# Optimization experiments

Hardware: AMD Instinct MI355X
Metric: run time of the kernel (lower is better)

## Reference

```python
import jax, jax.numpy as jnp
import numpy as np

B, M, K, D = 16384, 16, 256, 64
T = 1.0


def setup_inputs() -> dict:
    key = jax.random.key(0)
    k1, k2 = jax.random.split(key)
    x = jax.random.normal(k1, (B, M, D), dtype=jnp.float32)
    # nn.init.normal_(self.center, std=0.01)
    center = jax.random.normal(k2, (M, K, D), dtype=jnp.float32) * 0.01
    return {"x": x, "center": center}


def _forward(x, center):
    # x: [B, M, D]; center: [M, K, D]
    x1 = jax.lax.stop_gradient(x)              # x.detach() in the original
    x_sqlen = jnp.sum(x1 * x1, axis=-1)        # [B, M]
    dot = jnp.einsum('mkd,bmd->bmk', center, x1)  # bmm(center, x1) -> [B, M, K]
    c_sqlen = jnp.sum(center * center, axis=-1)   # [M, K]
    dist = c_sqlen[None, :, :] - 2.0 * dot + x_sqlen[:, :, None]  # [B, M, K]
    dist = -jnp.sqrt(dist)
    # softargmax with straight-through estimator
    y_soft = jax.nn.softmax(dist / T, axis=-1)
    label = jnp.argmax(y_soft, axis=-1, keepdims=True)            # [B, M, 1]
    y_hard = jax.nn.one_hot(label[..., 0], K, dtype=dist.dtype)   # [B, M, K]
    assign = y_hard - jax.lax.stop_gradient(y_soft) + y_soft
    # reconstruction: bmm(assign^T(M,B,K), center(M,K,D)) -> [B, M, D]
    recon = jnp.einsum('bmk,mkd->bmd', assign, center)
    return recon, center, label


def reference(x, center):
    return _forward(x, center)
```

## Files before the change

### kernel.cpp

```cpp
#include <hip/hip_runtime.h>
#include <stdint.h>
#include <math.h>

#define B_TOT 16384
#define M_TOT 16
#define K_TOT 256
#define D_TOT 64
#define ROWS_PB 256
#define THREADS 512
#define NCHUNK (B_TOT / ROWS_PB)
#define CAP 3072
#define XS 8.0e-3f
#define SLACK 5.0e-5f

typedef unsigned long long ull;
typedef __attribute__((ext_vector_type(8))) short short8;
typedef __attribute__((ext_vector_type(4))) float f32x4;
typedef __attribute__((ext_vector_type(4))) uint32_t u32x4;

__device__ __forceinline__ uint32_t f32_key(float f) {
  uint32_t u = __float_as_uint(f);
  return (u & 0x80000000u) ? ~u : (u | 0x80000000u);
}
__device__ __forceinline__ ull u64min(ull a, ull b) { return a < b ? a : b; }

__device__ __forceinline__ uint32_t bf16rne(float f) {
  uint32_t u = __float_as_uint(f);
  return (u + 0x7FFFu + ((u >> 16) & 1u)) >> 16;
}
__device__ __forceinline__ uint32_t pack2(float a, float b) {
  return bf16rne(a) | (bf16rne(b) << 16);
}

__device__ __forceinline__ int swz(int row, int c) {
  return row * 128 + ((c * 16) ^ ((row & 7) << 4));
}

__device__ __forceinline__ float xla_hsum16(const float* r) {
#pragma clang fp contract(off)
#pragma clang fp reassociate(off)
  float u[8];
#pragma unroll
  for (int q = 0; q < 8; ++q) u[q] = r[q] + r[q + 8];
  float v[4];
#pragma unroll
  for (int q = 0; q < 4; ++q) v[q] = u[q] + u[q + 4];
  float w0 = v[0] + v[2];
  float w1 = v[1] + v[3];
  return w0 + w1;
}

__device__ __forceinline__ ull exact_key_stream(int k, const float* __restrict__ xrow,
                                                const float* __restrict__ crow,
                                                float csq, float x_sq) {
#pragma clang fp contract(off)
#pragma clang fp reassociate(off)
  const float4* cp = reinterpret_cast<const float4*>(crow);
  const float4* xp = reinterpret_cast<const float4*>(xrow);
  float a[4] = {0.f, 0.f, 0.f, 0.f};
#pragma unroll
  for (int it = 0; it < 4; ++it) {
    float cc[16], xx[16];
#pragma unroll
    for (int q = 0; q < 4; ++q) {
      float4 v = cp[4 * it + q];
      cc[4 * q + 0] = v.x; cc[4 * q + 1] = v.y;
      cc[4 * q + 2] = v.z; cc[4 * q + 3] = v.w;
      float4 w = xp[4 * it + q];
      xx[4 * q + 0] = w.x; xx[4 * q + 1] = w.y;
      xx[4 * q + 2] = w.z; xx[4 * q + 3] = w.w;
    }
#pragma unroll
    for (int L = 0; L < 4; ++L) {
      float m3 = cc[12 + L] * xx[12 + L];
      float s3 = m3 + a[L];
      float m2 = cc[8 + L] * xx[8 + L];
      float s2 = m2 + s3;
      float m1 = cc[4 + L] * xx[4 + L];
      float s1 = m1 + s2;
      float m0 = cc[0 + L] * xx[0 + L];
      a[L] = m0 + s1;
    }
  }
  const float dot = (a[0] + a[1]) + (a[2] + a[3]);
  const float two_dot = 2.0f * dot;
  const float d2 = (csq - two_dot) + x_sq;
  const float s = (float)sqrt((double)d2);
  return (((ull)f32_key(s)) << 32) | (unsigned)k;
}

__global__ __launch_bounds__(THREADS, 4) void mkmeans_fwd(
    const float* __restrict__ x, const float* __restrict__ center,
    float* __restrict__ recon, float* __restrict__ outC, float* __restrict__ outL)
{
#pragma clang fp contract(off)
#pragma clang fp reassociate(off)
  __shared__ __align__(16) char s_cb[K_TOT * 128];
  __shared__ __align__(16) float s_csq[K_TOT];
  __shared__ __align__(16) float s_nch[K_TOT];
  __shared__ __align__(16) float s_csqrt[K_TOT];
  __shared__ float s_xsq[ROWS_PB];
  __shared__ float s_xnorm[ROWS_PB];
  __shared__ float s_cmaxw[4];
  __shared__ ull s_best[ROWS_PB];
  __shared__ uint32_t s_list[CAP];
  __shared__ int s_nc, s_ovf;

  const int t = threadIdx.x;
  const int l = t & 63;
  const int wv = t >> 6;
  const int g = l >> 4;
  const int j = l & 15;
  const int bi = blockIdx.x;
  const int m = bi & (M_TOT - 1);
  const int chunk = bi >> 4;
  const int b0 = chunk * ROWS_PB;

  const float* cmbase = center + (size_t)m * (K_TOT * D_TOT);

  if (t == 0) { s_nc = 0; s_ovf = 0; }

  if (t < ROWS_PB) {
    const float4* xp = reinterpret_cast<const float4*>(
        x + ((size_t)((b0 + t) * M_TOT + m)) * D_TOT);
    float r[16];
#pragma unroll
    for (int mm = 0; mm < 4; ++mm) {
      float q[16];
#pragma unroll
      for (int qq = 0; qq < 4; ++qq) {
        float4 v = xp[4 * mm + qq];
        q[4 * qq + 0] = v.x; q[4 * qq + 1] = v.y;
        q[4 * qq + 2] = v.z; q[4 * qq + 3] = v.w;
      }
#pragma unroll
      for (int jj = 0; jj < 16; ++jj) {
        const float p = q[jj] * q[jj];
        r[jj] = (mm == 0) ? p : (r[jj] + p);
      }
    }
    const float xsq = xla_hsum16(r);
    s_xsq[t] = xsq;
    s_xnorm[t] = sqrtf(xsq) * 1.00001f + 1e-12f;
    s_best[t] = ~0ull;
  } else {
    const int tc = t - ROWS_PB;
    const float4* cp = reinterpret_cast<const float4*>(cmbase + (size_t)tc * D_TOT);
    float4* dst = (chunk == 0)
        ? reinterpret_cast<float4*>(outC + (size_t)m * (K_TOT * D_TOT) + (size_t)tc * D_TOT)
        : nullptr;
    float r[16];
#pragma unroll
    for (int mm = 0; mm < 4; ++mm) {
      float q[16];
#pragma unroll
      for (int qq = 0; qq < 4; ++qq) {
        float4 v = cp[4 * mm + qq];
        if (dst) dst[4 * mm + qq] = v;
        q[4 * qq + 0] = v.x; q[4 * qq + 1] = v.y;
        q[4 * qq + 2] = v.z; q[4 * qq + 3] = v.w;
      }
#pragma unroll
      for (int jj = 0; jj < 16; ++jj) {
        const float p = q[jj] * q[jj];
        r[jj] = (mm == 0) ? p : (r[jj] + p);
      }
#pragma unroll
      for (int h = 0; h < 2; ++h) {
        u32x4 u = {pack2(q[8 * h + 0], q[8 * h + 1]),
                   pack2(q[8 * h + 2], q[8 * h + 3]),
                   pack2(q[8 * h + 4], q[8 * h + 5]),
                   pack2(q[8 * h + 6], q[8 * h + 7])};
        *reinterpret_cast<u32x4*>(s_cb + swz(tc, 2 * mm + h)) = u;
      }
    }
    const float csq = xla_hsum16(r);
    s_csq[tc] = csq;
    s_nch[tc] = -0.5f * csq;
    const float cs = sqrtf(csq) * 1.00001f + 1e-12f;
    s_csqrt[tc] = cs;
    float cw = cs;
#pragma unroll
    for (int off = 1; off < 64; off <<= 1)
      cw = fmaxf(cw, __shfl_xor(cw, off, 64));
    if (l == 0) s_cmaxw[wv - 4] = cw;
  }

  short8 bfr[2][2];
#pragma unroll
  for (int rg = 0; rg < 2; ++rg) {
    const int row = wv * 32 + rg * 16 + j;
    const float4* xr4 = reinterpret_cast<const float4*>(
        x + ((size_t)((b0 + row) * M_TOT + m)) * D_TOT);
#pragma unroll
    for (int ks = 0; ks < 2; ++ks) {
      const int c = ks * 4 + g;
      const float4 f0 = xr4[2 * c];
      const float4 f1 = xr4[2 * c + 1];
      u32x4 u = {pack2(f0.x, f0.y), pack2(f0.z, f0.w),
                 pack2(f1.x, f1.y), pack2(f1.z, f1.w)};
      bfr[rg][ks] = *reinterpret_cast<short8*>(&u);
    }
  }
  __syncthreads();

  float m1[2] = {-3.0e38f, -3.0e38f};
#pragma unroll
  for (int T = 0; T < 16; ++T) {
    const short8 af0 = *reinterpret_cast<const short8*>(s_cb + swz(T * 16 + j, g));
    const short8 af1 = *reinterpret_cast<const short8*>(s_cb + swz(T * 16 + j, 4 + g));
    const f32x4 nch = *reinterpret_cast<const f32x4*>(&s_nch[T * 16 + g * 4]);
#pragma unroll
    for (int rg = 0; rg < 2; ++rg) {
      f32x4 a = __builtin_amdgcn_mfma_f32_16x16x32_bf16(af0, bfr[rg][0], nch, 0, 0, 0);
      a = __builtin_amdgcn_mfma_f32_16x16x32_bf16(af1, bfr[rg][1], a, 0, 0, 0);
      m1[rg] = fmaxf(m1[rg], fmaxf(fmaxf(a[0], a[1]), fmaxf(a[2], a[3])));
    }
  }

  const float cmax = fmaxf(fmaxf(s_cmaxw[0], s_cmaxw[1]),
                           fmaxf(s_cmaxw[2], s_cmaxw[3]));
  float base[2], xw[2];
#pragma unroll
  for (int rg = 0; rg < 2; ++rg) {
    float v = m1[rg];
    v = fmaxf(v, __shfl_xor(v, 16, 64));
    v = fmaxf(v, __shfl_xor(v, 32, 64));
    xw[rg] = XS * s_xnorm[wv * 32 + rg * 16 + j];
    base[rg] = v - xw[rg] * cmax - SLACK;
  }

#pragma unroll
  for (int T = 0; T < 16; ++T) {
    const short8 af0 = *reinterpret_cast<const short8*>(s_cb + swz(T * 16 + j, g));
    const short8 af1 = *reinterpret_cast<const short8*>(s_cb + swz(T * 16 + j, 4 + g));
    const f32x4 nch = *reinterpret_cast<const f32x4*>(&s_nch[T * 16 + g * 4]);
    const f32x4 cs = *reinterpret_cast<const f32x4*>(&s_csqrt[T * 16 + g * 4]);
#pragma unroll
    for (int rg = 0; rg < 2; ++rg) {
      f32x4 a = __builtin_amdgcn_mfma_f32_16x16x32_bf16(af0, bfr[rg][0], nch, 0, 0, 0);
      a = __builtin_amdgcn_mfma_f32_16x16x32_bf16(af1, bfr[rg][1], a, 0, 0, 0);
      const int row = wv * 32 + rg * 16 + j;
#pragma unroll
      for (int i = 0; i < 4; ++i) {
        const float thr = fmaf(-xw[rg], cs[i], base[rg]);
        if (a[i] >= thr) {
          const int idx = atomicAdd(&s_nc, 1);
          if (idx < CAP)
            s_list[idx] = ((uint32_t)row << 16) | (uint32_t)(T * 16 + g * 4 + i);
          else
            s_ovf = 1;
        }
      }
    }
  }
  __syncthreads();

  if (!s_ovf) {
    const int n = s_nc;
#pragma unroll 1
    for (int i = t; i < n; i += THREADS) {
      const uint32_t e = s_list[i];
      const int row = (int)(e >> 16);
      const int k = (int)(e & 0xffffu);
      const float* xrow = x + ((size_t)((b0 + row) * M_TOT + m)) * D_TOT;
      const float* crow = cmbase + (size_t)k * D_TOT;
      const ull key = exact_key_stream(k, xrow, crow, s_csq[k], s_xsq[row]);
      atomicMin(&s_best[row], key);
    }
  } else if (t < ROWS_PB) {
    const float* xrow = x + ((size_t)((b0 + t) * M_TOT + m)) * D_TOT;
    ull best = ~0ull;
#pragma unroll 1
    for (int k = 0; k < K_TOT; ++k)
      best = u64min(best, exact_key_stream(k, xrow, cmbase + (size_t)k * D_TOT,
                                           s_csq[k], s_xsq[t]));
    s_best[t] = best;
  }
  __syncthreads();

  if (t < ROWS_PB)
    outL[(size_t)(b0 + t) * M_TOT + m] = (float)(uint32_t)(s_best[t] & 0xffffffffull);

  const float4* cm4 = reinterpret_cast<const float4*>(cmbase);
  float4* rec4 = reinterpret_cast<float4*>(recon);
#pragma unroll
  for (int it = 0; it < (ROWS_PB * 16) / THREADS; ++it) {
    const int slot = it * THREADS + t;
    const int row = slot >> 4, ch = slot & 15;
    const int kst = (int)(s_best[row] & 0xffffffffull);
    rec4[((size_t)((b0 + row) * M_TOT + m)) * 16 + ch] = cm4[kst * 16 + ch];
  }
}

extern "C" void kernel_launch(void* const* d_in, const int* in_sizes, int n_in,
                              void* d_out, int out_size, void* d_ws, size_t ws_size,
                              hipStream_t stream) {
  const float* x = (const float*)d_in[0];
  const float* center = (const float*)d_in[1];
  float* recon = (float*)d_out;
  float* outC = recon + (size_t)B_TOT * M_TOT * D_TOT;
  float* outL = outC + (size_t)M_TOT * K_TOT * D_TOT;

  mkmeans_fwd<<<dim3(NCHUNK * M_TOT), dim3(THREADS), 0, stream>>>(x, center, recon, outC, outL);
}
```

Baseline: 175.6 us.

## Fuse candidate filtering into single MFMA pass with bitmasks and wave-level compaction

Removes the second MFMA pass over all centroid tiles. During the single pass, each lane records a per-tile bitmask of entries within a uniform error bound of the tile max, plus a rounded-up bf16 copy of each tile max. After the row max is known, tiles whose max falls below the cut are dropped, and surviving candidates go into the list through a wave prefix sum with one atomic per wave instead of per-candidate atomics. The per-centroid norm-based threshold is replaced by a looser uniform bound using the max centroid norm, which may admit more candidates for exact rechecking. Occupancy hint drops from 4 to 3 to make room for the extra registers.

```diff
diff --git a/kernel.cpp b/kernel.cpp
--- a/kernel.cpp
+++ b/kernel.cpp
@@ -10,7 +10,7 @@
 #define THREADS 512
 #define NCHUNK (B_TOT / ROWS_PB)
 #define CAP 3072
-#define XS 8.0e-3f
+#define XERRF 0.0160f
 #define SLACK 5.0e-5f
 
 typedef unsigned long long ull;
@@ -30,6 +30,10 @@
 }
 __device__ __forceinline__ uint32_t pack2(float a, float b) {
   return bf16rne(a) | (bf16rne(b) << 16);
+}
+__device__ __forceinline__ uint32_t bf16up(float f) {
+  uint32_t u = __float_as_uint(f);
+  return (((int)u >= 0) ? (u + 0xFFFFu) : u) >> 16;
 }
 
 __device__ __forceinline__ int swz(int row, int c) {
@@ -89,7 +93,7 @@
   return (((ull)f32_key(s)) << 32) | (unsigned)k;
 }
 
-__global__ __launch_bounds__(THREADS, 4) void mkmeans_fwd(
+__global__ __launch_bounds__(THREADS, 3) void mkmeans_fwd(
     const float* __restrict__ x, const float* __restrict__ center,
     float* __restrict__ recon, float* __restrict__ outC, float* __restrict__ outL)
 {
@@ -98,7 +102,6 @@
   __shared__ __align__(16) char s_cb[K_TOT * 128];
   __shared__ __align__(16) float s_csq[K_TOT];
   __shared__ __align__(16) float s_nch[K_TOT];
-  __shared__ __align__(16) float s_csqrt[K_TOT];
   __shared__ float s_xsq[ROWS_PB];
   __shared__ float s_xnorm[ROWS_PB];
   __shared__ float s_cmaxw[4];
@@ -177,9 +180,7 @@
     const float csq = xla_hsum16(r);
     s_csq[tc] = csq;
     s_nch[tc] = -0.5f * csq;
-    const float cs = sqrtf(csq) * 1.00001f + 1e-12f;
-    s_csqrt[tc] = cs;
-    float cw = cs;
+    float cw = sqrtf(csq) * 1.00001f + 1e-12f;
 #pragma unroll
     for (int off = 1; off < 64; off <<= 1)
       cw = fmaxf(cw, __shfl_xor(cw, off, 64));
@@ -204,7 +205,16 @@
   }
   __syncthreads();
 
+  const float cmax = fmaxf(fmaxf(s_cmaxw[0], s_cmaxw[1]),
+                           fmaxf(s_cmaxw[2], s_cmaxw[3]));
+  float Wa[2];
+#pragma unroll
+  for (int rg = 0; rg < 2; ++rg)
+    Wa[rg] = XERRF * s_xnorm[wv * 32 + rg * 16 + j] * cmax + SLACK;
+
   float m1[2] = {-3.0e38f, -3.0e38f};
+  ull mk[2] = {0ull, 0ull};
+  uint32_t tb[2][8];
 #pragma unroll
   for (int T = 0; T < 16; ++T) {
     const short8 af0 = *reinterpret_cast<const short8*>(s_cb + swz(T * 16 + j, g));
@@ -214,44 +224,62 @@
     for (int rg = 0; rg < 2; ++rg) {
       f32x4 a = __builtin_amdgcn_mfma_f32_16x16x32_bf16(af0, bfr[rg][0], nch, 0, 0, 0);
       a = __builtin_amdgcn_mfma_f32_16x16x32_bf16(af1, bfr[rg][1], a, 0, 0, 0);
-      m1[rg] = fmaxf(m1[rg], fmaxf(fmaxf(a[0], a[1]), fmaxf(a[2], a[3])));
-    }
-  }
-
-  const float cmax = fmaxf(fmaxf(s_cmaxw[0], s_cmaxw[1]),
-                           fmaxf(s_cmaxw[2], s_cmaxw[3]));
-  float base[2], xw[2];
+      const float tmax = fmaxf(fmaxf(a[0], a[1]), fmaxf(a[2], a[3]));
+      const float thr = tmax - Wa[rg];
+      uint32_t bits = 0u;
+      bits |= (a[0] >= thr) ? 1u : 0u;
+      bits |= (a[1] >= thr) ? 2u : 0u;
+      bits |= (a[2] >= thr) ? 4u : 0u;
+      bits |= (a[3] >= thr) ? 8u : 0u;
+      mk[rg] |= ((ull)bits) << (4 * T);
+      m1[rg] = fmaxf(m1[rg], tmax);
+      const uint32_t h = bf16up(tmax);
+      if (T & 1) tb[rg][T >> 1] |= h << 16; else tb[rg][T >> 1] = h;
+    }
+  }
+
+  int cnt = 0;
 #pragma unroll
   for (int rg = 0; rg < 2; ++rg) {
     float v = m1[rg];
     v = fmaxf(v, __shfl_xor(v, 16, 64));
     v = fmaxf(v, __shfl_xor(v, 32, 64));
-    xw[rg] = XS * s_xnorm[wv * 32 + rg * 16 + j];
-    base[rg] = v - xw[rg] * cmax - SLACK;
-  }
-
-#pragma unroll
-  for (int T = 0; T < 16; ++T) {
-    const short8 af0 = *reinterpret_cast<const short8*>(s_cb + swz(T * 16 + j, g));
-    const short8 af1 = *reinterpret_cast<const short8*>(s_cb + swz(T * 16 + j, 4 + g));
-    const f32x4 nch = *reinterpret_cast<const f32x4*>(&s_nch[T * 16 + g * 4]);
-    const f32x4 cs = *reinterpret_cast<const f32x4*>(&s_csqrt[T * 16 + g * 4]);
-#pragma unroll
-    for (int rg = 0; rg < 2; ++rg) {
-      f32x4 a = __builtin_amdgcn_mfma_f32_16x16x32_bf16(af0, bfr[rg][0], nch, 0, 0, 0);
-      a = __builtin_amdgcn_mfma_f32_16x16x32_bf16(af1, bfr[rg][1], a, 0, 0, 0);
-      const int row = wv * 32 + rg * 16 + j;
-#pragma unroll
-      for (int i = 0; i < 4; ++i) {
-        const float thr = fmaf(-xw[rg], cs[i], base[rg]);
-        if (a[i] >= thr) {
-          const int idx = atomicAdd(&s_nc, 1);
-          if (idx < CAP)
-            s_list[idx] = ((uint32_t)row << 16) | (uint32_t)(T * 16 + g * 4 + i);
-          else
-            s_ovf = 1;
-        }
-      }
+    const float cut = v - Wa[rg];
+    ull fm = 0ull;
+#pragma unroll
+    for (int T = 0; T < 16; ++T) {
+      const uint32_t h = (tb[rg][T >> 1] >> ((T & 1) * 16)) & 0xFFFFu;
+      const float tmaxbf = __uint_as_float(h << 16);
+      if (tmaxbf >= cut)
+        fm |= (mk[rg] >> (4 * T) & 0xFull) << (4 * T);
+    }
+    mk[rg] = fm;
+    cnt += __popcll(fm);
+  }
+
+  int pre = cnt;
+#pragma unroll
+  for (int off = 1; off < 64; off <<= 1) {
+    const int v = __shfl_up(pre, off, 64);
+    if (l >= off) pre += v;
+  }
+  int base = 0;
+  if (l == 63) base = atomicAdd(&s_nc, pre);
+  base = __shfl(base, 63, 64);
+  int pos = base + pre - cnt;
+#pragma unroll
+  for (int rg = 0; rg < 2; ++rg) {
+    const int row = wv * 32 + rg * 16 + j;
+    ull msk = mk[rg];
+    while (msk) {
+      const int p = __builtin_ctzll(msk);
+      msk &= msk - 1;
+      const int k = (p >> 2) * 16 + g * 4 + (p & 3);
+      if (pos < CAP)
+        s_list[pos] = ((uint32_t)row << 16) | (uint32_t)k;
+      else
+        s_ovf = 1;
+      ++pos;
     }
   }
   __syncthreads();
```

Result: slower. 186.6 us (+6.3%).
